# Kernel optimization log

Measured on AMD Instinct MI355X. Metric: run time of the kernel, lower is better.

The kernel has to match this reference:

```python
import jax, jax.numpy as jnp
import numpy as np

H, G, D = 16, 4, 2048          # num_heads, num_groups, hidden_dim
HD = D // H                     # head_dim = 128
KV = G * HD                     # kv proj dim = 512


def setup_inputs() -> dict:
    key = jax.random.key(0)
    ks = jax.random.split(key, 9)
    sc = 0.02
    X = jax.random.normal(ks[0], (2, 2048, D), dtype=jnp.float32)
    Wq = jax.random.normal(ks[1], (D, D), dtype=jnp.float32) * sc
    bq = jnp.zeros((D,), dtype=jnp.float32)
    Wk = jax.random.normal(ks[2], (D, KV), dtype=jnp.float32) * sc
    bk = jnp.zeros((KV,), dtype=jnp.float32)
    Wv = jax.random.normal(ks[3], (D, KV), dtype=jnp.float32) * sc
    bv = jnp.zeros((KV,), dtype=jnp.float32)
    Wo = jax.random.normal(ks[4], (D, D), dtype=jnp.float32) * sc
    bo = jnp.zeros((D,), dtype=jnp.float32)
    return {"X": X, "Wq": Wq, "bq": bq, "Wk": Wk, "bk": bk,
            "Wv": Wv, "bv": bv, "Wo": Wo, "bo": bo}


def _expand_kv(t, bs, s):
    # Faithful replication of the torch code: reshape->unsqueeze->expand->reshape.
    # (bs, s, G, HD) -> (bs, s, 1, G, HD) -> (bs, s, H//G, G, HD) -> reshape (bs, H, s, HD)
    # This raw row-major reshape (NOT a transpose) is exactly what the source does.
    t = t.reshape(bs, s, G, HD)
    t = jnp.broadcast_to(t[:, :, None, :, :], (bs, s, H // G, G, HD))
    return t.reshape(bs, H, s, HD)


def reference(X, Wq, bq, Wk, bk, Wv, bv, Wo, bo):
    bs, s, d = X.shape
    q = (X @ Wq + bq).reshape(bs, s, H, HD).transpose(0, 2, 1, 3)  # [bs,H,s,HD]
    k = _expand_kv(X @ Wk + bk, bs, s)                              # [bs,H,s,HD]
    v = _expand_kv(X @ Wv + bv, bs, s)                              # [bs,H,s,HD]
    scale = jnp.asarray(HD, X.dtype) ** 0.5
    scores = jnp.einsum('bhqd,bhkd->bhqk', q, k) / scale            # [bs,H,s,s]
    mask = jnp.tril(jnp.ones((s, s), dtype=bool))[None, None]
    scores = jnp.where(mask, scores, -jnp.inf)
    attn = jax.nn.softmax(scores, axis=-1)
    out = jnp.einsum('bhqk,bhkd->bhqd', attn, v)                    # [bs,H,s,HD]
    out = out.transpose(0, 2, 1, 3).reshape(bs, s, d)
    return out @ Wo + bo
```

## Files before the change

### kernel.cpp

```cpp
#include <hip/hip_runtime.h>


#define DEV __device__ __forceinline__

typedef float f32x4 __attribute__((ext_vector_type(4)));
typedef __bf16 bf16x8 __attribute__((ext_vector_type(8)));

DEV f32x4 mfma16(bf16x8 a, bf16x8 b, f32x4 c) {
  return __builtin_amdgcn_mfma_f32_16x16x32_bf16(a, b, c, 0, 0, 0);
}

DEV void gld16(const void* gsrc, void* ldst) {
  __builtin_amdgcn_global_load_lds(
      (const __attribute__((address_space(1))) unsigned int*)gsrc,
      (__attribute__((address_space(3))) unsigned int*)ldst, 16, 0, 0);
}

__global__ void convert_f32_bf16(const float* __restrict__ in, __bf16* __restrict__ out) {
  size_t i = ((size_t)blockIdx.x * 256 + threadIdx.x) * 8;
  float4 a = *(const float4*)(in + i);
  float4 b = *(const float4*)(in + i + 4);
  bf16x8 v;
  v[0] = (__bf16)a.x; v[1] = (__bf16)a.y; v[2] = (__bf16)a.z; v[3] = (__bf16)a.w;
  v[4] = (__bf16)b.x; v[5] = (__bf16)b.y; v[6] = (__bf16)b.z; v[7] = (__bf16)b.w;
  *(bf16x8*)(out + i) = v;
}

__global__ void transpose_w_bf16(const float* __restrict__ W, __bf16* __restrict__ WT,
                                 int K, int N) {
  __shared__ float t[32][33];
  int tx = threadIdx.x & 31, ty = threadIdx.x >> 5;
  int n0 = blockIdx.x * 32, k0 = blockIdx.y * 32;
#pragma unroll
  for (int i = 0; i < 4; i++)
    t[ty + i * 8][tx] = W[(size_t)(k0 + ty + i * 8) * N + n0 + tx];
  __syncthreads();
#pragma unroll
  for (int i = 0; i < 4; i++)
    WT[(size_t)(n0 + ty + i * 8) * K + k0 + tx] = (__bf16)t[tx][ty + i * 8];
}

template <int F32OUT>
__global__ __launch_bounds__(256, 3)
void gemm_bt(const __bf16* __restrict__ A, const __bf16* __restrict__ Bt,
             const float* __restrict__ bias, float scale, void* __restrict__ Cout,
             int M, int N, int K) {
  __shared__ __bf16 As[128 * 32];
  __shared__ __bf16 Bs[128 * 32];
  int tid = threadIdx.x, lane = tid & 63, w = tid >> 6;
  int wm = w >> 1, wn = w & 1, lg = lane >> 4, lc = lane & 15;
  int m0 = blockIdx.y * 128, n0 = blockIdx.x * 128;
  int srow = w * 16 + (lane >> 2), scol = (lane & 3) * 8;
  const __bf16* Ag = A + (size_t)(m0 + srow) * K + scol;
  const __bf16* Bg = Bt + (size_t)(n0 + srow) * K + scol;
  f32x4 acc[4][4] = {};
  int nk = K >> 5;
  for (int kt = 0; kt < nk; ++kt) {
    if (kt) __syncthreads();
    const __bf16* a = Ag + kt * 32;
    const __bf16* bp = Bg + kt * 32;
    gld16((void*)a, As + (w * 16) * 32);
    gld16((void*)(a + (size_t)64 * K), As + (64 + w * 16) * 32);
    gld16((void*)bp, Bs + (w * 16) * 32);
    gld16((void*)(bp + (size_t)64 * K), Bs + (64 + w * 16) * 32);
    __syncthreads();
    bf16x8 af[4], bf[4];
#pragma unroll
    for (int i = 0; i < 4; i++)
      af[i] = *(const bf16x8*)(As + (wm * 64 + i * 16 + lc) * 32 + lg * 8);
#pragma unroll
    for (int i = 0; i < 4; i++)
      bf[i] = *(const bf16x8*)(Bs + (wn * 64 + i * 16 + lc) * 32 + lg * 8);
#pragma unroll
    for (int mi = 0; mi < 4; mi++)
#pragma unroll
      for (int ni = 0; ni < 4; ni++)
        acc[mi][ni] = mfma16(af[mi], bf[ni], acc[mi][ni]);
  }
  float bcol[4];
#pragma unroll
  for (int ni = 0; ni < 4; ni++) bcol[ni] = bias[n0 + wn * 64 + ni * 16 + lc];
#pragma unroll
  for (int mi = 0; mi < 4; mi++)
#pragma unroll
    for (int ni = 0; ni < 4; ni++)
#pragma unroll
      for (int r = 0; r < 4; r++) {
        int row = m0 + wm * 64 + mi * 16 + lg * 4 + r;
        int col = n0 + wn * 64 + ni * 16 + lc;
        float v = (acc[mi][ni][r] + bcol[ni]) * scale;
        if (F32OUT)
          ((float*)Cout)[(size_t)row * N + col] = v;
        else
          ((__bf16*)Cout)[(size_t)row * N + col] = (__bf16)v;
      }
}

__global__ __launch_bounds__(256, 3)
void gemm_qkv(const __bf16* __restrict__ A, const __bf16* __restrict__ Bt,
              const float* __restrict__ bq, const float* __restrict__ bk,
              const float* __restrict__ bv, float qscale,
              __bf16* __restrict__ Qo, __bf16* __restrict__ Ko, __bf16* __restrict__ Vo) {
  const int K = 2048;
  __shared__ __bf16 As[128 * 32];
  __shared__ __bf16 Bs[128 * 32];
  int tid = threadIdx.x, lane = tid & 63, w = tid >> 6;
  int wm = w >> 1, wn = w & 1, lg = lane >> 4, lc = lane & 15;
  int m0 = blockIdx.y * 128, n0 = blockIdx.x * 128;
  int srow = w * 16 + (lane >> 2), scol = (lane & 3) * 8;
  const __bf16* Ag = A + (size_t)(m0 + srow) * K + scol;
  const __bf16* Bg = Bt + (size_t)(n0 + srow) * K + scol;
  f32x4 acc[4][4] = {};
  for (int kt = 0; kt < 64; ++kt) {
    if (kt) __syncthreads();
    const __bf16* a = Ag + kt * 32;
    const __bf16* bp = Bg + kt * 32;
    gld16((void*)a, As + (w * 16) * 32);
    gld16((void*)(a + (size_t)64 * K), As + (64 + w * 16) * 32);
    gld16((void*)bp, Bs + (w * 16) * 32);
    gld16((void*)(bp + (size_t)64 * K), Bs + (64 + w * 16) * 32);
    __syncthreads();
    bf16x8 af[4], bf[4];
#pragma unroll
    for (int i = 0; i < 4; i++)
      af[i] = *(const bf16x8*)(As + (wm * 64 + i * 16 + lc) * 32 + lg * 8);
#pragma unroll
    for (int i = 0; i < 4; i++)
      bf[i] = *(const bf16x8*)(Bs + (wn * 64 + i * 16 + lc) * 32 + lg * 8);
#pragma unroll
    for (int mi = 0; mi < 4; mi++)
#pragma unroll
      for (int ni = 0; ni < 4; ni++)
        acc[mi][ni] = mfma16(af[mi], bf[ni], acc[mi][ni]);
  }
  const float* bp;
  __bf16* op;
  int ldc, c0;
  float scl;
  if (n0 < 2048) { bp = bq; op = Qo; ldc = 2048; c0 = n0; scl = qscale; }
  else if (n0 < 2560) { bp = bk; op = Ko; ldc = 512; c0 = n0 - 2048; scl = 1.f; }
  else { bp = bv; op = Vo; ldc = 512; c0 = n0 - 2560; scl = 1.f; }
  float bcol[4];
#pragma unroll
  for (int ni = 0; ni < 4; ni++) bcol[ni] = bp[c0 + wn * 64 + ni * 16 + lc];
#pragma unroll
  for (int mi = 0; mi < 4; mi++)
#pragma unroll
    for (int ni = 0; ni < 4; ni++)
#pragma unroll
      for (int r = 0; r < 4; r++) {
        int row = m0 + wm * 64 + mi * 16 + lg * 4 + r;
        int col = c0 + wn * 64 + ni * 16 + lc;
        op[(size_t)row * ldc + col] = (__bf16)((acc[mi][ni][r] + bcol[ni]) * scl);
      }
}

__global__ void expand_vc(const __bf16* __restrict__ Vp, __bf16* __restrict__ Vc) {
  __shared__ __bf16 Vl[8][512];
  int tid = threadIdx.x;
  int kt = blockIdx.x, bh = blockIdx.y, b = bh >> 4, h = bh & 15;
  size_t base = (size_t)b * 2048 + h * 128 + kt * 8;
#pragma unroll
  for (int i = 0; i < 2; ++i) {
    int idx = i * 256 + tid;
    int rr = idx >> 6, ch = idx & 63;
    *(float4*)(&Vl[rr][ch * 8]) = *(const float4*)(Vp + (base + rr) * 512 + ch * 8);
  }
  __syncthreads();
  __bf16* out = Vc + ((size_t)(bh * 16 + kt)) * 4096;
#pragma unroll
  for (int i = 0; i < 2; ++i) {
    int u = i * 256 + tid;
    int d = u >> 2, m = u & 3;
    int seg = m ^ ((d >> 1) & 3);
    bf16x8 val;
#pragma unroll
    for (int j = 0; j < 8; j++) val[j] = Vl[j][seg * 128 + d];
    *(bf16x8*)(out + u * 8) = val;
  }
}

__global__ __launch_bounds__(512, 4)
void attn_fwd(const __bf16* __restrict__ Qb, const __bf16* __restrict__ Kp,
              const __bf16* __restrict__ VcG, __bf16* __restrict__ attO) {
  __shared__ alignas(16) char Kl[2][8192];
  __shared__ alignas(16) char Vld[2][8192];
  int tid = threadIdx.x, lane = tid & 63, w = tid >> 6;
  int lg = lane >> 4, lc = lane & 15;
  int slot = (int)blockIdx.y;
  int qt = (slot < 8) ? (15 - 2 * slot) : (2 * slot - 16);
  int bh = blockIdx.x, b = bh >> 4, h = bh & 15;
  int q0 = qt * 128;
  int qg = q0 + w * 16 + lc;
  const __bf16* Qrow = Qb + (size_t)(b * 2048 + qg) * 2048 + h * 128 + lg * 8;
  bf16x8 qf[4];
#pragma unroll
  for (int ks = 0; ks < 4; ks++) qf[ks] = *(const bf16x8*)(Qrow + ks * 32);
  asm volatile("s_waitcnt vmcnt(0)" ::: "memory");
  f32x4 o[8] = {};
  float mrow = -3.0e38f, lsum = 0.f;
  const char* KpB = (const char*)Kp + (size_t)(b * 2048 + h * 128) * 1024;
  const char* VgB = (const char*)VcG + (size_t)bh * 16 * 8192;
  int ktmax = qt;
  int ksw = (lane * 16) ^ ((lane >> 4) << 5);
  int seg = lc >> 2;
  int kro = seg * 256;
  int lg16 = lg * 16;
  int kswr[4];
#pragma unroll
  for (int ks = 0; ks < 4; ks++) kswr[ks] = (ks * 64 + lg16) ^ (seg << 5);
  int vbase = lc * 64 + (lg16 ^ ((lc & 6) << 3));

#define STAGE(bufi, ktile)                                                             \
  do {                                                                                 \
    gld16(KpB + (size_t)((ktile) * 8 + w) * 1024 + ksw, &Kl[bufi][w * 1024]);          \
    gld16(VgB + (size_t)(ktile) * 8192 + w * 1024 + lane * 16, &Vld[bufi][w * 1024]);  \
  } while (0)

  int cur = 0;
  STAGE(0, 0);
  for (int kt = 0; kt <= ktmax; ++kt) {
    if (kt < ktmax) {
      STAGE(cur ^ 1, kt + 1);
      asm volatile("s_waitcnt vmcnt(2)" ::: "memory");
    } else {
      asm volatile("s_waitcnt vmcnt(0)" ::: "memory");
    }
    __builtin_amdgcn_s_barrier();
    const char* Kc = Kl[cur];
    const char* Vc = Vld[cur];

    f32x4 s[8];
    __builtin_amdgcn_s_setprio(1);
#pragma unroll
    for (int nt = 0; nt < 8; nt++) {
      if (kt * 128 + nt * 16 <= q0 + w * 16 + 15) {
        s[nt] = (f32x4){0.f, 0.f, 0.f, 0.f};
#pragma unroll
        for (int ks = 0; ks < 4; ks++) {
          bf16x8 kf = *(const bf16x8*)(Kc + nt * 1024 + kro + kswr[ks]);
          s[nt] = mfma16(kf, qf[ks], s[nt]);
        }
      } else {
        s[nt] = (f32x4){-3.0e38f, -3.0e38f, -3.0e38f, -3.0e38f};
      }
    }
    __builtin_amdgcn_s_setprio(0);
    if (kt == ktmax) {
#pragma unroll
      for (int nt = 0; nt < 8; nt++)
#pragma unroll
        for (int r = 0; r < 4; r++)
          if (kt * 128 + nt * 16 + r * 4 + lg > qg) s[nt][r] = -3.0e38f;
    }
    float v = fmaxf(fmaxf(s[0][0], s[0][1]), fmaxf(s[0][2], s[0][3]));
#pragma unroll
    for (int nt = 1; nt < 8; nt++)
      v = fmaxf(v, fmaxf(fmaxf(s[nt][0], s[nt][1]), fmaxf(s[nt][2], s[nt][3])));
    v = fmaxf(v, __shfl_xor(v, 16));
    v = fmaxf(v, __shfl_xor(v, 32));
    if (__any(v > mrow + 8.0f)) {
      float mn = fmaxf(mrow, v);
      float sc = exp2f(mrow - mn);
      mrow = mn;
      lsum *= sc;
#pragma unroll
      for (int r = 0; r < 4; r++) {
        float scr = __shfl(sc, lg * 4 + r);
#pragma unroll
        for (int dt = 0; dt < 8; dt++) o[dt][r] *= scr;
      }
    }
    float pf[8];
    float rs = 0.f;
#pragma unroll
    for (int nt = 0; nt < 8; nt++) {
      float e0 = exp2f(s[nt][0] - mrow);
      float e1 = exp2f(s[nt][1] - mrow);
      float e2 = exp2f(s[nt][2] - mrow);
      float e3 = exp2f(s[nt][3] - mrow);
      pf[nt] = (e0 + e1) + (e2 + e3);
      rs += pf[nt];
    }
    lsum += rs;
    bf16x8 af;
#pragma unroll
    for (int j = 0; j < 8; j++) af[j] = (__bf16)pf[j];
    __builtin_amdgcn_s_setprio(1);
#pragma unroll
    for (int dt = 0; dt < 8; dt++) {
      bf16x8 vf = *(const bf16x8*)(Vc + dt * 1024 + vbase);
      o[dt] = mfma16(af, vf, o[dt]);
    }
    __builtin_amdgcn_s_setprio(0);
    __builtin_amdgcn_s_barrier();
    cur ^= 1;
  }
  lsum += __shfl_xor(lsum, 16);
  lsum += __shfl_xor(lsum, 32);
  float inv = 1.0f / lsum;
#pragma unroll
  for (int r = 0; r < 4; r++) {
    float invr = __shfl(inv, lg * 4 + r);
    int row = b * 2048 + q0 + w * 16 + lg * 4 + r;
#pragma unroll
    for (int dt = 0; dt < 8; dt++)
      attO[(size_t)row * 2048 + h * 128 + dt * 16 + lc] = (__bf16)(o[dt][r] * invr);
  }
#undef STAGE
}

extern "C" void kernel_launch(void* const* d_in, const int* in_sizes, int n_in,
                              void* d_out, int out_size, void* d_ws, size_t ws_size,
                              hipStream_t stream) {
  const float* X = (const float*)d_in[0];
  const float* Wq = (const float*)d_in[1];
  const float* bq = (const float*)d_in[2];
  const float* Wk = (const float*)d_in[3];
  const float* bk = (const float*)d_in[4];
  const float* Wv = (const float*)d_in[5];
  const float* bv = (const float*)d_in[6];
  const float* Wo = (const float*)d_in[7];
  const float* bo = (const float*)d_in[8];
  char* ws = (char*)d_ws;
  const size_t MB = 1024 * 1024;
  __bf16* Xb     = (__bf16*)(ws + 0);
  __bf16* WqkvT  = (__bf16*)(ws + 16 * MB);
  __bf16* WoT    = (__bf16*)(ws + 28 * MB);
  __bf16* Qbf    = (__bf16*)(ws + 36 * MB);
  __bf16* Kp     = (__bf16*)(ws + 52 * MB);
  __bf16* Vp     = (__bf16*)(ws + 56 * MB);
  __bf16* Vc     = (__bf16*)(ws + 60 * MB);
  __bf16* aO     = (__bf16*)(ws + 64 * MB);

  convert_f32_bf16<<<4096, 256, 0, stream>>>(X, Xb);
  transpose_w_bf16<<<dim3(64, 64), 256, 0, stream>>>(Wq, WqkvT, 2048, 2048);
  transpose_w_bf16<<<dim3(16, 64), 256, 0, stream>>>(Wk, WqkvT + (size_t)2048 * 2048, 2048, 512);
  transpose_w_bf16<<<dim3(16, 64), 256, 0, stream>>>(Wv, WqkvT + (size_t)2560 * 2048, 2048, 512);
  transpose_w_bf16<<<dim3(64, 64), 256, 0, stream>>>(Wo, WoT, 2048, 2048);

  float qscale = 1.4426950408889634f * 0.08838834764831845f;
  gemm_qkv<<<dim3(24, 32), 256, 0, stream>>>(Xb, WqkvT, bq, bk, bv, qscale, Qbf, Kp, Vp);

  expand_vc<<<dim3(16, 32), 256, 0, stream>>>(Vp, Vc);
  attn_fwd<<<dim3(32, 16), 512, 0, stream>>>(Qbf, Kp, Vc, aO);

  gemm_bt<1><<<dim3(16, 32), 256, 0, stream>>>(aO, WoT, bo, 1.0f, (float*)d_out, 4096, 2048, 2048);
}
```

Measured before the change: 287.9 us.

## Merge prep kernels, swizzle GEMM LDS reads, fuse V expansion into QKV GEMM

Combines the X conversion and four weight transposes into one launch. Applies an XOR swizzle to the LDS staging columns in both GEMMs to reduce bank conflicts on fragment reads. Writes V directly into the swizzled per-head layout from the QKV GEMM epilogue, which removes the expand_vc kernel and the intermediate Vp buffer. The trade-off is a more complex epilogue with scattered 8-byte stores.

```diff
diff --git a/kernel.cpp b/kernel.cpp
--- a/kernel.cpp
+++ b/kernel.cpp
@@ -5,6 +5,7 @@
 
 typedef float f32x4 __attribute__((ext_vector_type(4)));
 typedef __bf16 bf16x8 __attribute__((ext_vector_type(8)));
+typedef __bf16 bf16x4 __attribute__((ext_vector_type(4)));
 
 DEV f32x4 mfma16(bf16x8 a, bf16x8 b, f32x4 c) {
   return __builtin_amdgcn_mfma_f32_16x16x32_bf16(a, b, c, 0, 0, 0);
@@ -16,28 +17,38 @@
       (__attribute__((address_space(3))) unsigned int*)ldst, 16, 0, 0);
 }
 
-__global__ void convert_f32_bf16(const float* __restrict__ in, __bf16* __restrict__ out) {
-  size_t i = ((size_t)blockIdx.x * 256 + threadIdx.x) * 8;
-  float4 a = *(const float4*)(in + i);
-  float4 b = *(const float4*)(in + i + 4);
-  bf16x8 v;
-  v[0] = (__bf16)a.x; v[1] = (__bf16)a.y; v[2] = (__bf16)a.z; v[3] = (__bf16)a.w;
-  v[4] = (__bf16)b.x; v[5] = (__bf16)b.y; v[6] = (__bf16)b.z; v[7] = (__bf16)b.w;
-  *(bf16x8*)(out + i) = v;
-}
-
-__global__ void transpose_w_bf16(const float* __restrict__ W, __bf16* __restrict__ WT,
-                                 int K, int N) {
+__global__ void prep(const float* __restrict__ X, __bf16* __restrict__ Xb,
+                     const float* __restrict__ Wq, const float* __restrict__ Wk,
+                     const float* __restrict__ Wv, const float* __restrict__ Wo,
+                     __bf16* __restrict__ WqkvT, __bf16* __restrict__ WoT) {
   __shared__ float t[32][33];
-  int tx = threadIdx.x & 31, ty = threadIdx.x >> 5;
-  int n0 = blockIdx.x * 32, k0 = blockIdx.y * 32;
+  int id = blockIdx.x, tid = threadIdx.x;
+  if (id < 4096) {
+    size_t i = ((size_t)id * 256 + tid) * 8;
+    float4 a = *(const float4*)(X + i);
+    float4 b = *(const float4*)(X + i + 4);
+    bf16x8 v;
+    v[0] = (__bf16)a.x; v[1] = (__bf16)a.y; v[2] = (__bf16)a.z; v[3] = (__bf16)a.w;
+    v[4] = (__bf16)b.x; v[5] = (__bf16)b.y; v[6] = (__bf16)b.z; v[7] = (__bf16)b.w;
+    *(bf16x8*)(Xb + i) = v;
+    return;
+  }
+  const float* W;
+  __bf16* WT;
+  int N, nx, ky;
+  if (id < 8192) { int r = id - 4096; W = Wq; WT = WqkvT; N = 2048; nx = r & 63; ky = r >> 6; }
+  else if (id < 9216) { int r = id - 8192; W = Wk; WT = WqkvT + (size_t)2048 * 2048; N = 512; nx = r & 15; ky = r >> 4; }
+  else if (id < 10240) { int r = id - 9216; W = Wv; WT = WqkvT + (size_t)2560 * 2048; N = 512; nx = r & 15; ky = r >> 4; }
+  else { int r = id - 10240; W = Wo; WT = WoT; N = 2048; nx = r & 63; ky = r >> 6; }
+  int tx = tid & 31, ty = tid >> 5;
+  int n0 = nx * 32, k0 = ky * 32;
 #pragma unroll
   for (int i = 0; i < 4; i++)
     t[ty + i * 8][tx] = W[(size_t)(k0 + ty + i * 8) * N + n0 + tx];
   __syncthreads();
 #pragma unroll
   for (int i = 0; i < 4; i++)
-    WT[(size_t)(n0 + ty + i * 8) * K + k0 + tx] = (__bf16)t[tx][ty + i * 8];
+    WT[(size_t)(n0 + ty + i * 8) * 2048 + k0 + tx] = (__bf16)t[tx][ty + i * 8];
 }
 
 template <int F32OUT>
@@ -50,9 +61,11 @@
   int tid = threadIdx.x, lane = tid & 63, w = tid >> 6;
   int wm = w >> 1, wn = w & 1, lg = lane >> 4, lc = lane & 15;
   int m0 = blockIdx.y * 128, n0 = blockIdx.x * 128;
-  int srow = w * 16 + (lane >> 2), scol = (lane & 3) * 8;
+  int srow = w * 16 + (lane >> 2);
+  int scol = ((lane & 3) ^ ((lane >> 2) & 3)) * 8;
   const __bf16* Ag = A + (size_t)(m0 + srow) * K + scol;
   const __bf16* Bg = Bt + (size_t)(n0 + srow) * K + scol;
+  int rdA = lg ^ (lc & 3);
   f32x4 acc[4][4] = {};
   int nk = K >> 5;
   for (int kt = 0; kt < nk; ++kt) {
@@ -67,10 +80,10 @@
     bf16x8 af[4], bf[4];
 #pragma unroll
     for (int i = 0; i < 4; i++)
-      af[i] = *(const bf16x8*)(As + (wm * 64 + i * 16 + lc) * 32 + lg * 8);
+      af[i] = *(const bf16x8*)(As + (wm * 64 + i * 16 + lc) * 32 + rdA * 8);
 #pragma unroll
     for (int i = 0; i < 4; i++)
-      bf[i] = *(const bf16x8*)(Bs + (wn * 64 + i * 16 + lc) * 32 + lg * 8);
+      bf[i] = *(const bf16x8*)(Bs + (wn * 64 + i * 16 + lc) * 32 + rdA * 8);
 #pragma unroll
     for (int mi = 0; mi < 4; mi++)
 #pragma unroll
@@ -100,16 +113,18 @@
 void gemm_qkv(const __bf16* __restrict__ A, const __bf16* __restrict__ Bt,
               const float* __restrict__ bq, const float* __restrict__ bk,
               const float* __restrict__ bv, float qscale,
-              __bf16* __restrict__ Qo, __bf16* __restrict__ Ko, __bf16* __restrict__ Vo) {
+              __bf16* __restrict__ Qo, __bf16* __restrict__ Ko, __bf16* __restrict__ Vc) {
   const int K = 2048;
   __shared__ __bf16 As[128 * 32];
   __shared__ __bf16 Bs[128 * 32];
   int tid = threadIdx.x, lane = tid & 63, w = tid >> 6;
   int wm = w >> 1, wn = w & 1, lg = lane >> 4, lc = lane & 15;
   int m0 = blockIdx.y * 128, n0 = blockIdx.x * 128;
-  int srow = w * 16 + (lane >> 2), scol = (lane & 3) * 8;
+  int srow = w * 16 + (lane >> 2);
+  int scol = ((lane & 3) ^ ((lane >> 2) & 3)) * 8;
   const __bf16* Ag = A + (size_t)(m0 + srow) * K + scol;
   const __bf16* Bg = Bt + (size_t)(n0 + srow) * K + scol;
+  int rdA = lg ^ (lc & 3);
   f32x4 acc[4][4] = {};
   for (int kt = 0; kt < 64; ++kt) {
     if (kt) __syncthreads();
@@ -123,60 +138,66 @@
     bf16x8 af[4], bf[4];
 #pragma unroll
     for (int i = 0; i < 4; i++)
-      af[i] = *(const bf16x8*)(As + (wm * 64 + i * 16 + lc) * 32 + lg * 8);
+      af[i] = *(const bf16x8*)(As + (wm * 64 + i * 16 + lc) * 32 + rdA * 8);
 #pragma unroll
     for (int i = 0; i < 4; i++)
-      bf[i] = *(const bf16x8*)(Bs + (wn * 64 + i * 16 + lc) * 32 + lg * 8);
+      bf[i] = *(const bf16x8*)(Bs + (wn * 64 + i * 16 + lc) * 32 + rdA * 8);
 #pragma unroll
     for (int mi = 0; mi < 4; mi++)
 #pragma unroll
       for (int ni = 0; ni < 4; ni++)
         acc[mi][ni] = mfma16(af[mi], bf[ni], acc[mi][ni]);
   }
-  const float* bp;
-  __bf16* op;
-  int ldc, c0;
-  float scl;
-  if (n0 < 2048) { bp = bq; op = Qo; ldc = 2048; c0 = n0; scl = qscale; }
-  else if (n0 < 2560) { bp = bk; op = Ko; ldc = 512; c0 = n0 - 2048; scl = 1.f; }
-  else { bp = bv; op = Vo; ldc = 512; c0 = n0 - 2560; scl = 1.f; }
-  float bcol[4];
-#pragma unroll
-  for (int ni = 0; ni < 4; ni++) bcol[ni] = bp[c0 + wn * 64 + ni * 16 + lc];
-#pragma unroll
-  for (int mi = 0; mi < 4; mi++)
-#pragma unroll
-    for (int ni = 0; ni < 4; ni++)
-#pragma unroll
-      for (int r = 0; r < 4; r++) {
-        int row = m0 + wm * 64 + mi * 16 + lg * 4 + r;
+  if (n0 < 2048) {
+    float bcol[4];
+#pragma unroll
+    for (int ni = 0; ni < 4; ni++) bcol[ni] = bq[n0 + wn * 64 + ni * 16 + lc];
+#pragma unroll
+    for (int mi = 0; mi < 4; mi++)
+#pragma unroll
+      for (int ni = 0; ni < 4; ni++)
+#pragma unroll
+        for (int r = 0; r < 4; r++) {
+          int row = m0 + wm * 64 + mi * 16 + lg * 4 + r;
+          int col = n0 + wn * 64 + ni * 16 + lc;
+          Qo[(size_t)row * 2048 + col] = (__bf16)((acc[mi][ni][r] + bcol[ni]) * qscale);
+        }
+  } else if (n0 < 2560) {
+    int c0 = n0 - 2048;
+    float bcol[4];
+#pragma unroll
+    for (int ni = 0; ni < 4; ni++) bcol[ni] = bk[c0 + wn * 64 + ni * 16 + lc];
+#pragma unroll
+    for (int mi = 0; mi < 4; mi++)
+#pragma unroll
+      for (int ni = 0; ni < 4; ni++)
+#pragma unroll
+        for (int r = 0; r < 4; r++) {
+          int row = m0 + wm * 64 + mi * 16 + lg * 4 + r;
+          int col = c0 + wn * 64 + ni * 16 + lc;
+          Ko[(size_t)row * 512 + col] = (__bf16)(acc[mi][ni][r] + bcol[ni]);
+        }
+  } else {
+    int c0 = n0 - 2560;
+    int by = blockIdx.y;
+    float bcol[4];
+#pragma unroll
+    for (int ni = 0; ni < 4; ni++) bcol[ni] = bv[c0 + wn * 64 + ni * 16 + lc];
+#pragma unroll
+    for (int mi = 0; mi < 4; mi++) {
+      int lrbase = wm * 64 + mi * 16 + lg * 4;
+      int kt = lrbase >> 3, j0 = lrbase & 7;
+#pragma unroll
+      for (int ni = 0; ni < 4; ni++) {
         int col = c0 + wn * 64 + ni * 16 + lc;
-        op[(size_t)row * ldc + col] = (__bf16)((acc[mi][ni][r] + bcol[ni]) * scl);
+        int seg = col >> 7, d = col & 127;
+        bf16x4 pk;
+#pragma unroll
+        for (int r = 0; r < 4; r++) pk[r] = (__bf16)(acc[mi][ni][r] + bcol[ni]);
+        size_t e = (size_t)(by * 16 + kt) * 4096 + (d * 4 + (seg ^ ((d >> 1) & 3))) * 8 + j0;
+        *(bf16x4*)(Vc + e) = pk;
       }
-}
-
-__global__ void expand_vc(const __bf16* __restrict__ Vp, __bf16* __restrict__ Vc) {
-  __shared__ __bf16 Vl[8][512];
-  int tid = threadIdx.x;
-  int kt = blockIdx.x, bh = blockIdx.y, b = bh >> 4, h = bh & 15;
-  size_t base = (size_t)b * 2048 + h * 128 + kt * 8;
-#pragma unroll
-  for (int i = 0; i < 2; ++i) {
-    int idx = i * 256 + tid;
-    int rr = idx >> 6, ch = idx & 63;
-    *(float4*)(&Vl[rr][ch * 8]) = *(const float4*)(Vp + (base + rr) * 512 + ch * 8);
-  }
-  __syncthreads();
-  __bf16* out = Vc + ((size_t)(bh * 16 + kt)) * 4096;
-#pragma unroll
-  for (int i = 0; i < 2; ++i) {
-    int u = i * 256 + tid;
-    int d = u >> 2, m = u & 3;
-    int seg = m ^ ((d >> 1) & 3);
-    bf16x8 val;
-#pragma unroll
-    for (int j = 0; j < 8; j++) val[j] = Vl[j][seg * 128 + d];
-    *(bf16x8*)(out + u * 8) = val;
+    }
   }
 }
 
@@ -329,20 +350,14 @@
   __bf16* WoT    = (__bf16*)(ws + 28 * MB);
   __bf16* Qbf    = (__bf16*)(ws + 36 * MB);
   __bf16* Kp     = (__bf16*)(ws + 52 * MB);
-  __bf16* Vp     = (__bf16*)(ws + 56 * MB);
-  __bf16* Vc     = (__bf16*)(ws + 60 * MB);
-  __bf16* aO     = (__bf16*)(ws + 64 * MB);
-
-  convert_f32_bf16<<<4096, 256, 0, stream>>>(X, Xb);
-  transpose_w_bf16<<<dim3(64, 64), 256, 0, stream>>>(Wq, WqkvT, 2048, 2048);
-  transpose_w_bf16<<<dim3(16, 64), 256, 0, stream>>>(Wk, WqkvT + (size_t)2048 * 2048, 2048, 512);
-  transpose_w_bf16<<<dim3(16, 64), 256, 0, stream>>>(Wv, WqkvT + (size_t)2560 * 2048, 2048, 512);
-  transpose_w_bf16<<<dim3(64, 64), 256, 0, stream>>>(Wo, WoT, 2048, 2048);
+  __bf16* Vc     = (__bf16*)(ws + 56 * MB);
+  __bf16* aO     = (__bf16*)(ws + 60 * MB);
+
+  prep<<<14336, 256, 0, stream>>>(X, Xb, Wq, Wk, Wv, Wo, WqkvT, WoT);
 
   float qscale = 1.4426950408889634f * 0.08838834764831845f;
-  gemm_qkv<<<dim3(24, 32), 256, 0, stream>>>(Xb, WqkvT, bq, bk, bv, qscale, Qbf, Kp, Vp);
-
-  expand_vc<<<dim3(16, 32), 256, 0, stream>>>(Vp, Vc);
+  gemm_qkv<<<dim3(24, 32), 256, 0, stream>>>(Xb, WqkvT, bq, bk, bv, qscale, Qbf, Kp, Vc);
+
   attn_fwd<<<dim3(32, 16), 512, 0, stream>>>(Qbf, Kp, Vc, aO);
 
   gemm_bt<1><<<dim3(16, 32), 256, 0, stream>>>(aO, WoT, bo, 1.0f, (float*)d_out, 4096, 2048, 2048);
```

After: 278.0 us. 3.4% less time.
